# Kernel optimization log

Measured on AMD Instinct MI355X. Metric: run time of the kernel, lower is better.

The kernel has to match this reference:

```python
import jax, jax.numpy as jnp
import numpy as np

B, H, S, D = 4, 16, 2048, 64

def setup_inputs() -> dict:
    key = jax.random.key(0)
    kq, kk, kv = jax.random.split(key, 3)
    Q = jax.random.normal(kq, (B, H, S, D), dtype=jnp.float32)
    K = jax.random.normal(kk, (B, H, S, D), dtype=jnp.float32)
    V = jax.random.normal(kv, (B, H, S, D), dtype=jnp.float32)
    return {"Q": Q, "K": K, "V": V}

def reference(Q, K, V):
    # Faithful to the source: NO 1/sqrt(d) scaling.
    # scores: [B, H, S, S]
    scores = jnp.einsum("bhqd,bhkd->bhqk", Q, K)
    probs = jax.nn.softmax(scores, axis=-1)
    # output: [B, H, S, D]
    return jnp.einsum("bhqk,bhkd->bhqd", probs, V)
```

## Files before the change

kernel.cpp:

```cpp
#include <hip/hip_runtime.h>
#include <hip/hip_bf16.h>
#include <math.h>

typedef _Float16 f16x8 __attribute__((ext_vector_type(8)));
typedef _Float16 f16x4 __attribute__((ext_vector_type(4)));
typedef __fp16   hf4  __attribute__((ext_vector_type(4)));
typedef float    f32x4 __attribute__((ext_vector_type(4)));
typedef __bf16   bf16x8 __attribute__((ext_vector_type(8)));
typedef __bf16   bf16x4 __attribute__((ext_vector_type(4)));

#define MFMA32_F16(a,b,c)  __builtin_amdgcn_mfma_f32_16x16x32_f16((a),(b),(c),0,0,0)
#define MFMA_BF16(a,b,c)   __builtin_amdgcn_mfma_f32_16x16x32_bf16((a),(b),(c),0,0,0)

constexpr int S_LEN = 2048;
constexpr int DH    = 64;
constexpr int KBLK  = 64;
constexpr int NSTEP = S_LEN / KBLK;
constexpr float LOG2E = 1.44269504088896340736f;
constexpr size_t TILE_BYTES = 16384;
constexpr size_t WS_NEED = 64ull * NSTEP * TILE_BYTES;

__device__ __forceinline__ void gload16(const void* g, void* l) {
    __builtin_amdgcn_global_load_lds(
        (const __attribute__((address_space(1))) void*)g,
        (__attribute__((address_space(3))) void*)l, 16, 0, 0);
}

__device__ __forceinline__ float exp2_fast(float x) {
    float r;
    asm("v_exp_f32 %0, %1" : "=v"(r) : "v"(x));
    return r;
}

__device__ __forceinline__ float redmax_lg(float x) {
    x = fmaxf(x, __shfl_xor(x, 16));
    x = fmaxf(x, __shfl_xor(x, 32));
    return x;
}
__device__ __forceinline__ float redadd_lg(float x) {
    x += __shfl_xor(x, 16);
    x += __shfl_xor(x, 32);
    return x;
}

__device__ __forceinline__ f16x4 as_f16x4(hf4 h) {
    f16x4 f;
    __builtin_memcpy(&f, &h, 8);
    return f;
}

__global__ __launch_bounds__(256)
void prep_kernel(const float* __restrict__ Kg, const float* __restrict__ Vg,
                 unsigned char* __restrict__ ws)
{
    __shared__ _Float16 sT[64 * 70];

    const int blk = blockIdx.x;
    const int tid = threadIdx.x;
    const float* Kt = Kg + (size_t)blk * KBLK * DH;
    const float* Vt = Vg + (size_t)blk * KBLK * DH;
    char* wK = (char*)(ws + (size_t)blk * TILE_BYTES);
    char* wV = wK + 8192;

    #pragma unroll
    for (int c = 0; c < 2; ++c) {
        const int eid = tid + c * 256;
        const int row = eid >> 3;
        const int d0  = (eid & 7) * 8;
        f32x4 a = *(const f32x4*)(Kt + row * DH + d0);
        f32x4 b = *(const f32x4*)(Kt + row * DH + d0 + 4);
        f16x8 h;
        #pragma unroll
        for (int j = 0; j < 4; ++j) { h[j] = (_Float16)a[j]; h[4 + j] = (_Float16)b[j]; }
        const int koff = (row * 128 + d0 * 2) ^ ((row & 7) << 4);
        *(f16x8*)(wK + koff) = h;
        f32x4 va = *(const f32x4*)(Vt + row * DH + d0);
        f32x4 vb = *(const f32x4*)(Vt + row * DH + d0 + 4);
        #pragma unroll
        for (int j = 0; j < 4; ++j) {
            sT[row * 70 + d0 + j]     = (_Float16)va[j];
            sT[row * 70 + d0 + 4 + j] = (_Float16)vb[j];
        }
    }
    __syncthreads();
    #pragma unroll
    for (int c = 0; c < 2; ++c) {
        const int id  = tid + c * 256;
        const int p   = id >> 8;
        const int lgc = (id >> 6) & 3;
        const int d   = id & 63;
        const int kv0 = p * 32 + lgc * 4;
        f16x8 h;
        #pragma unroll
        for (int j = 0; j < 4; ++j) {
            h[j]     = sT[(kv0 + j) * 70 + d];
            h[4 + j] = sT[(kv0 + 16 + j) * 70 + d];
        }
        *(f16x8*)(wV + (p * 4 + lgc) * 1024 + d * 16) = h;
    }
}

__global__ __launch_bounds__(256, 4)
void attn_main(const float* __restrict__ Qg0, const unsigned char* __restrict__ ws,
               float* __restrict__ Og0)
{
    __shared__ __align__(16) _Float16 sK[2][KBLK * DH];
    __shared__ __align__(16) _Float16 sV[2][KBLK * DH];

    const int tid  = threadIdx.x;
    const int lane = tid & 63;
    const int w    = tid >> 6;
    const int lg   = lane >> 4;
    const int li   = lane & 15;
    const int X    = (li & 7) << 4;

    const int n   = blockIdx.x;
    const int xcd = n & 7;
    const int m_  = n >> 3;
    const int bh  = xcd * 8 + (m_ >> 4);
    const int qp  = m_ & 15;

    const float* Qg = Qg0 + (size_t)bh * S_LEN * DH;
    float*       Og = Og0 + (size_t)bh * S_LEN * DH;
    const unsigned char* wsb = ws + (size_t)bh * NSTEP * TILE_BYTES;

    f16x8 qA[2], qB[2];
    {
        const int qrowA = qp * 128 + w * 16 + li;
        const float* pa = Qg + (size_t)qrowA * DH;
        const float* pb = pa + 64 * DH;
        #pragma unroll
        for (int f = 0; f < 2; ++f) {
            f32x4 a0 = *(const f32x4*)(pa + f * 32 + lg * 8);
            f32x4 a1 = *(const f32x4*)(pa + f * 32 + lg * 8 + 4);
            f32x4 b0 = *(const f32x4*)(pb + f * 32 + lg * 8);
            f32x4 b1 = *(const f32x4*)(pb + f * 32 + lg * 8 + 4);
            #pragma unroll
            for (int j = 0; j < 4; ++j) {
                qA[f][j]     = (_Float16)(a0[j] * LOG2E);
                qA[f][4 + j] = (_Float16)(a1[j] * LOG2E);
                qB[f][j]     = (_Float16)(b0[j] * LOG2E);
                qB[f][4 + j] = (_Float16)(b1[j] * LOG2E);
            }
        }
    }

    f32x4 accoA[4], accoB[4];
    #pragma unroll
    for (int t = 0; t < 4; ++t) {
        accoA[t] = f32x4{0.f, 0.f, 0.f, 0.f};
        accoB[t] = f32x4{0.f, 0.f, 0.f, 0.f};
    }
    float mA = 0.f, lA = 0.f, mB = 0.f, lB = 0.f;

    auto stage = [&](int buf, int t) {
        const unsigned char* src = wsb + (size_t)t * TILE_BYTES;
        char* lk = (char*)&sK[buf][0] + w * 2048;
        char* lv = (char*)&sV[buf][0] + w * 2048;
        const unsigned char* gk = src + w * 2048 + lane * 16;
        const unsigned char* gv = src + 8192 + w * 2048 + lane * 16;
        gload16(gk,        lk);
        gload16(gk + 1024, lk + 1024);
        gload16(gv,        lv);
        gload16(gv + 1024, lv + 1024);
    };

    stage(0, 0);
    __syncthreads();
    int buf = 0;

    for (int t = 0; t < NSTEP; ++t) {
        if (t + 1 < NSTEP) stage(buf ^ 1, t + 1);

        const char* kb = (const char*)&sK[buf][0];
        const char* vb = (const char*)&sV[buf][0];

        f32x4 sA[4], sB[4];
        const f32x4 cA = {-mA, -mA, -mA, -mA};
        const f32x4 cB = {-mB, -mB, -mB, -mB};
        __builtin_amdgcn_s_setprio(1);
        #pragma unroll
        for (int t4 = 0; t4 < 4; ++t4) {
            const char* kr = kb + t4 * 2048 + li * 128;
            f16x8 kf0 = *(const f16x8*)(kr + ((0 * 64 + lg * 16) ^ X));
            f16x8 kf1 = *(const f16x8*)(kr + ((1 * 64 + lg * 16) ^ X));
            f32x4 a = MFMA32_F16(kf0, qA[0], cA);
            a       = MFMA32_F16(kf1, qA[1], a);
            f32x4 b = MFMA32_F16(kf0, qB[0], cB);
            b       = MFMA32_F16(kf1, qB[1], b);
            sA[t4] = a;
            sB[t4] = b;
        }
        __builtin_amdgcn_s_setprio(0);

        float mlA = fmaxf(fmaxf(fmaxf(sA[0][0], sA[0][1]), sA[0][2]),
                          fmaxf(fmaxf(sA[0][3], sA[1][0]), sA[1][1]));
        mlA = fmaxf(mlA, fmaxf(fmaxf(sA[1][2], sA[1][3]), sA[2][0]));
        mlA = fmaxf(mlA, fmaxf(fmaxf(sA[2][1], sA[2][2]), sA[2][3]));
        mlA = fmaxf(mlA, fmaxf(fmaxf(sA[3][0], sA[3][1]), fmaxf(sA[3][2], sA[3][3])));
        float mlB = fmaxf(fmaxf(fmaxf(sB[0][0], sB[0][1]), sB[0][2]),
                          fmaxf(fmaxf(sB[0][3], sB[1][0]), sB[1][1]));
        mlB = fmaxf(mlB, fmaxf(fmaxf(sB[1][2], sB[1][3]), sB[2][0]));
        mlB = fmaxf(mlB, fmaxf(fmaxf(sB[2][1], sB[2][2]), sB[2][3]));
        mlB = fmaxf(mlB, fmaxf(fmaxf(sB[3][0], sB[3][1]), fmaxf(sB[3][2], sB[3][3])));

        if (__any(mlA > 8.f)) {
            const float rowmax = redmax_lg(mlA);
            const float delta  = fmaxf(rowmax, 0.f);
            const float sc     = exp2_fast(-delta);
            mA += delta;  lA *= sc;
            #pragma unroll
            for (int t4 = 0; t4 < 4; ++t4) { accoA[t4] *= sc; sA[t4] -= delta; }
        }
        if (__any(mlB > 8.f)) {
            const float rowmax = redmax_lg(mlB);
            const float delta  = fmaxf(rowmax, 0.f);
            const float sc     = exp2_fast(-delta);
            mB += delta;  lB *= sc;
            #pragma unroll
            for (int t4 = 0; t4 < 4; ++t4) { accoB[t4] *= sc; sB[t4] -= delta; }
        }

        f16x4 pA[4], pB[4];
        float suA = 0.f, suB = 0.f;
        #pragma unroll
        for (int t4 = 0; t4 < 4; ++t4) {
            float a0 = exp2_fast(sA[t4][0]);
            float a1 = exp2_fast(sA[t4][1]);
            float a2 = exp2_fast(sA[t4][2]);
            float a3 = exp2_fast(sA[t4][3]);
            suA += (a0 + a1) + (a2 + a3);
            pA[t4] = as_f16x4(__builtin_shufflevector(
                __builtin_amdgcn_cvt_pkrtz(a0, a1),
                __builtin_amdgcn_cvt_pkrtz(a2, a3), 0, 1, 2, 3));
            float b0 = exp2_fast(sB[t4][0]);
            float b1 = exp2_fast(sB[t4][1]);
            float b2 = exp2_fast(sB[t4][2]);
            float b3 = exp2_fast(sB[t4][3]);
            suB += (b0 + b1) + (b2 + b3);
            pB[t4] = as_f16x4(__builtin_shufflevector(
                __builtin_amdgcn_cvt_pkrtz(b0, b1),
                __builtin_amdgcn_cvt_pkrtz(b2, b3), 0, 1, 2, 3));
        }
        lA += suA;
        lB += suB;

        __builtin_amdgcn_s_setprio(1);
        #pragma unroll
        for (int p = 0; p < 2; ++p) {
            f16x8 pfA = __builtin_shufflevector(pA[2 * p], pA[2 * p + 1], 0, 1, 2, 3, 4, 5, 6, 7);
            f16x8 pfB = __builtin_shufflevector(pB[2 * p], pB[2 * p + 1], 0, 1, 2, 3, 4, 5, 6, 7);
            #pragma unroll
            for (int t4v = 0; t4v < 4; ++t4v) {
                f16x8 vv = *(const f16x8*)(vb + p * 4096 + lg * 1024 + t4v * 256 + li * 16);
                accoA[t4v] = MFMA32_F16(vv, pfA, accoA[t4v]);
                accoB[t4v] = MFMA32_F16(vv, pfB, accoB[t4v]);
            }
        }
        __builtin_amdgcn_s_setprio(0);

        __syncthreads();
        buf ^= 1;
    }

    {
        const float ltotA = redadd_lg(lA);
        const float ltotB = redadd_lg(lB);
        const int qrowA = qp * 128 + w * 16 + li;
        const float ia = 1.f / ltotA;
        const float ib = 1.f / ltotB;
        float* oa = Og + (size_t)qrowA * DH;
        float* ob = oa + 64 * DH;
        #pragma unroll
        for (int t4 = 0; t4 < 4; ++t4) {
            f32x4 o1, o2;
            #pragma unroll
            for (int r = 0; r < 4; ++r) { o1[r] = accoA[t4][r] * ia; o2[r] = accoB[t4][r] * ib; }
            *(f32x4*)(oa + t4 * 16 + lg * 4) = o1;
            *(f32x4*)(ob + t4 * 16 + lg * 4) = o2;
        }
    }
}

__global__ __launch_bounds__(256)
void attn_fwd_kernel(const float* __restrict__ Qg0,
                     const float* __restrict__ Kg0,
                     const float* __restrict__ Vg0,
                     float* __restrict__ Og0)
{
    constexpr int VT_P = 72;
    constexpr int P_PB = 72;
    __shared__ __align__(16) __bf16 sKh[KBLK * DH];
    __shared__ __align__(16) __bf16 sKl[KBLK * DH];
    __shared__ __align__(16) __bf16 sVt[DH * VT_P];
    __shared__ __align__(16) __bf16 sP[4][16 * P_PB];

    const int tid  = threadIdx.x;
    const int lane = tid & 63;
    const int w    = tid >> 6;
    const int lg   = lane >> 4;
    const int li   = lane & 15;

    const int n   = blockIdx.x;
    const int xcd = n & 7;
    const int m   = n >> 3;
    const int bh  = xcd * 8 + (m >> 5);
    const int qt  = m & 31;

    const float* Qg = Qg0 + (size_t)bh * S_LEN * DH;
    const float* Kg = Kg0 + (size_t)bh * S_LEN * DH;
    const float* Vg = Vg0 + (size_t)bh * S_LEN * DH;
    float*       Og = Og0 + (size_t)bh * S_LEN * DH;

    bf16x8 qh[2], ql[2];
    {
        const int qrow = qt * 64 + w * 16 + li;
        const float* qp = Qg + (size_t)qrow * DH;
        #pragma unroll
        for (int f = 0; f < 2; ++f) {
            const int dbase = f * 32 + lg * 8;
            #pragma unroll
            for (int j = 0; j < 8; ++j) {
                float q = qp[dbase + j];
                __bf16 h = (__bf16)q;
                qh[f][j] = h;
                ql[f][j] = (__bf16)(q - (float)h);
            }
        }
    }

    f32x4 acco[4];
    #pragma unroll
    for (int t = 0; t < 4; ++t) acco[t] = f32x4{0.f, 0.f, 0.f, 0.f};
    float mval[4], lval[4];
    #pragma unroll
    for (int r = 0; r < 4; ++r) { mval[r] = -INFINITY; lval[r] = 0.f; }

    for (int step = 0; step < NSTEP; ++step) {
        __syncthreads();
        {
            const int kv0 = step * KBLK;
            #pragma unroll
            for (int i = 0; i < 4; ++i) {
                const int f4 = tid + i * 256;
                const int kv = f4 >> 4;
                const int d4 = (f4 & 15) << 2;
                f32x4 kvec = *(const f32x4*)(Kg + (size_t)(kv0 + kv) * DH + d4);
                bf16x4 h, l;
                #pragma unroll
                for (int j = 0; j < 4; ++j) {
                    __bf16 hh = (__bf16)kvec[j];
                    h[j] = hh;
                    l[j] = (__bf16)(kvec[j] - (float)hh);
                }
                const int idx = (kv * DH + d4) ^ ((kv & 7) << 3);
                *(bf16x4*)&sKh[idx] = h;
                *(bf16x4*)&sKl[idx] = l;
                f32x4 vvec = *(const f32x4*)(Vg + (size_t)(kv0 + kv) * DH + d4);
                #pragma unroll
                for (int j = 0; j < 4; ++j)
                    sVt[(d4 + j) * VT_P + kv] = (__bf16)vvec[j];
            }
        }
        __syncthreads();

        f32x4 accs[4];
        #pragma unroll
        for (int t4 = 0; t4 < 4; ++t4) {
            f32x4 acc = f32x4{0.f, 0.f, 0.f, 0.f};
            const int row = t4 * 16 + li;
            #pragma unroll
            for (int f = 0; f < 2; ++f) {
                const int idx = (row * DH + f * 32 + lg * 8) ^ ((row & 7) << 3);
                bf16x8 kh = *(const bf16x8*)&sKh[idx];
                bf16x8 kl = *(const bf16x8*)&sKl[idx];
                acc = MFMA_BF16(qh[f], kh, acc);
                acc = MFMA_BF16(qh[f], kl, acc);
                acc = MFMA_BF16(ql[f], kh, acc);
            }
            accs[t4] = acc;
        }

        #pragma unroll
        for (int r = 0; r < 4; ++r) {
            float mx = fmaxf(fmaxf(accs[0][r], accs[1][r]), fmaxf(accs[2][r], accs[3][r]));
            #pragma unroll
            for (int msk = 1; msk <= 8; msk <<= 1)
                mx = fmaxf(mx, __shfl_xor(mx, msk));
            const float newm  = fmaxf(mval[r], mx);
            const float scale = __expf(mval[r] - newm);
            mval[r] = newm;
            lval[r] *= scale;
            #pragma unroll
            for (int t4 = 0; t4 < 4; ++t4) acco[t4][r] *= scale;
            float s = 0.f;
            #pragma unroll
            for (int t4 = 0; t4 < 4; ++t4) {
                float p = __expf(accs[t4][r] - newm);
                accs[t4][r] = p;
                s += p;
            }
            #pragma unroll
            for (int msk = 1; msk <= 8; msk <<= 1)
                s += __shfl_xor(s, msk);
            lval[r] += s;
        }

        #pragma unroll
        for (int r = 0; r < 4; ++r) {
            const int rr = lg * 4 + r;
            #pragma unroll
            for (int t4 = 0; t4 < 4; ++t4)
                sP[w][rr * P_PB + t4 * 16 + li] = (__bf16)accs[t4][r];
        }

        bf16x8 pa[2];
        #pragma unroll
        for (int f = 0; f < 2; ++f)
            pa[f] = *(const bf16x8*)&sP[w][li * P_PB + f * 32 + lg * 8];
        #pragma unroll
        for (int t4 = 0; t4 < 4; ++t4) {
            #pragma unroll
            for (int f = 0; f < 2; ++f) {
                bf16x8 vb = *(const bf16x8*)&sVt[(t4 * 16 + li) * VT_P + f * 32 + lg * 8];
                acco[t4] = MFMA_BF16(pa[f], vb, acco[t4]);
            }
        }
    }

    {
        const int qrow0 = qt * 64 + w * 16;
        #pragma unroll
        for (int r = 0; r < 4; ++r) {
            const int rr = lg * 4 + r;
            const float inv = 1.f / lval[r];
            #pragma unroll
            for (int t4 = 0; t4 < 4; ++t4)
                Og[(size_t)(qrow0 + rr) * DH + t4 * 16 + li] = acco[t4][r] * inv;
        }
    }
}

extern "C" void kernel_launch(void* const* d_in, const int* in_sizes, int n_in,
                              void* d_out, int out_size, void* d_ws, size_t ws_size,
                              hipStream_t stream) {
    const float* Q = (const float*)d_in[0];
    const float* K = (const float*)d_in[1];
    const float* V = (const float*)d_in[2];
    float* O = (float*)d_out;
    if (ws_size >= WS_NEED) {
        prep_kernel<<<dim3(2048), dim3(256), 0, stream>>>(K, V, (unsigned char*)d_ws);
        attn_main<<<dim3(1024), dim3(256), 0, stream>>>(Q, (const unsigned char*)d_ws, O);
    } else {
        attn_fwd_kernel<<<dim3(2048), dim3(256), 0, stream>>>(Q, K, V, O);
    }
}
```

Before: 102.6 us.

## Software-pipeline attention loop to overlap QK^T of next tile with PV of previous

Splits the per-tile body into qkt, softmax, loadv and pv stages and reorders the loop so that each iteration computes QK^T for tile t, then PV for tile t-1, then softmax for tile t. The V fragments and packed probabilities are carried in registers across iterations, and a prologue and epilogue handle the first and last tiles. The aim is to interleave MFMA work with the exp and max softmax work so the matrix unit is less idle. In exchange it holds extra V and P registers live across iterations, which raises VGPR pressure and may reduce occupancy. The loop is also unrolled by two.

```diff
diff --git a/kernel.cpp b/kernel.cpp
--- a/kernel.cpp
+++ b/kernel.cpp
@@ -165,17 +165,10 @@
         gload16(gv + 1024, lv + 1024);
     };
 
-    stage(0, 0);
-    __syncthreads();
-    int buf = 0;
-
-    for (int t = 0; t < NSTEP; ++t) {
-        if (t + 1 < NSTEP) stage(buf ^ 1, t + 1);
-
-        const char* kb = (const char*)&sK[buf][0];
-        const char* vb = (const char*)&sV[buf][0];
-
-        f32x4 sA[4], sB[4];
+    f16x8 vprev[8];
+    f16x8 pfAprev[2], pfBprev[2];
+
+    auto qkt = [&](const char* kb, f32x4* sA, f32x4* sB) {
         const f32x4 cA = {-mA, -mA, -mA, -mA};
         const f32x4 cB = {-mB, -mB, -mB, -mB};
         __builtin_amdgcn_s_setprio(1);
@@ -192,7 +185,9 @@
             sB[t4] = b;
         }
         __builtin_amdgcn_s_setprio(0);
-
+    };
+
+    auto softmax = [&](f32x4* sA, f32x4* sB, f16x8* pfA, f16x8* pfB) {
         float mlA = fmaxf(fmaxf(fmaxf(sA[0][0], sA[0][1]), sA[0][2]),
                           fmaxf(fmaxf(sA[0][3], sA[1][0]), sA[1][1]));
         mlA = fmaxf(mlA, fmaxf(fmaxf(sA[1][2], sA[1][3]), sA[2][0]));
@@ -244,25 +239,71 @@
         }
         lA += suA;
         lB += suB;
-
+        #pragma unroll
+        for (int p = 0; p < 2; ++p) {
+            pfA[p] = __builtin_shufflevector(pA[2 * p], pA[2 * p + 1], 0, 1, 2, 3, 4, 5, 6, 7);
+            pfB[p] = __builtin_shufflevector(pB[2 * p], pB[2 * p + 1], 0, 1, 2, 3, 4, 5, 6, 7);
+        }
+    };
+
+    auto loadv = [&](const char* vb, f16x8* vv) {
+        #pragma unroll
+        for (int p = 0; p < 2; ++p)
+            #pragma unroll
+            for (int t4v = 0; t4v < 4; ++t4v)
+                vv[p * 4 + t4v] = *(const f16x8*)(vb + p * 4096 + lg * 1024 + t4v * 256 + li * 16);
+    };
+
+    auto pv = [&](const f16x8* vv, const f16x8* pfA, const f16x8* pfB) {
         __builtin_amdgcn_s_setprio(1);
         #pragma unroll
         for (int p = 0; p < 2; ++p) {
-            f16x8 pfA = __builtin_shufflevector(pA[2 * p], pA[2 * p + 1], 0, 1, 2, 3, 4, 5, 6, 7);
-            f16x8 pfB = __builtin_shufflevector(pB[2 * p], pB[2 * p + 1], 0, 1, 2, 3, 4, 5, 6, 7);
             #pragma unroll
             for (int t4v = 0; t4v < 4; ++t4v) {
-                f16x8 vv = *(const f16x8*)(vb + p * 4096 + lg * 1024 + t4v * 256 + li * 16);
-                accoA[t4v] = MFMA32_F16(vv, pfA, accoA[t4v]);
-                accoB[t4v] = MFMA32_F16(vv, pfB, accoB[t4v]);
+                accoA[t4v] = MFMA32_F16(vv[p * 4 + t4v], pfA[p], accoA[t4v]);
+                accoB[t4v] = MFMA32_F16(vv[p * 4 + t4v], pfB[p], accoB[t4v]);
             }
         }
         __builtin_amdgcn_s_setprio(0);
+    };
+
+    stage(0, 0);
+    __syncthreads();
+    int buf = 0;
+    {
+        stage(1, 1);
+        f32x4 sA[4], sB[4];
+        qkt((const char*)&sK[0][0], sA, sB);
+        loadv((const char*)&sV[0][0], vprev);
+        softmax(sA, sB, pfAprev, pfBprev);
+        __syncthreads();
+        buf = 1;
+    }
+
+    #pragma unroll 2
+    for (int t = 1; t < NSTEP; ++t) {
+        if (t + 1 < NSTEP) stage(buf ^ 1, t + 1);
+
+        f32x4 sA[4], sB[4];
+        qkt((const char*)&sK[buf][0], sA, sB);
+        pv(vprev, pfAprev, pfBprev);
+
+        f16x8 vcur[8];
+        loadv((const char*)&sV[buf][0], vcur);
+
+        f16x8 pfA[2], pfB[2];
+        softmax(sA, sB, pfA, pfB);
+
+        #pragma unroll
+        for (int i = 0; i < 8; ++i) vprev[i] = vcur[i];
+        pfAprev[0] = pfA[0]; pfAprev[1] = pfA[1];
+        pfBprev[0] = pfB[0]; pfBprev[1] = pfB[1];
 
         __syncthreads();
         buf ^= 1;
     }
 
+    pv(vprev, pfAprev, pfBprev);
     {
         const float ltotA = redadd_lg(lA);
         const float ltotB = redadd_lg(lB);
```

Result: slower. 311.3 us (+203.5%).

## Software-pipeline PV of previous tile with QK of current tile

Applied to the files above, without the earlier changes.

Restructures the attention loop so each iteration runs the P·V MFMAs for the previous key block right after the Q·K MFMAs for the current block. The softmax exponentials are then computed after both matrix phases, so the two MFMA phases can overlap with the exp/max work. V gets a third LDS buffer so the previous tile's V stays resident while the next one is being staged, and a prologue and epilogue handle the first and last tiles. This raises LDS use per block and keeps the P fragments alive across iterations, which costs registers and could lower occupancy.

```diff
diff --git a/kernel.cpp b/kernel.cpp
--- a/kernel.cpp
+++ b/kernel.cpp
@@ -105,7 +105,7 @@
                float* __restrict__ Og0)
 {
     __shared__ __align__(16) _Float16 sK[2][KBLK * DH];
-    __shared__ __align__(16) _Float16 sV[2][KBLK * DH];
+    __shared__ __align__(16) _Float16 sV[3][KBLK * DH];
 
     const int tid  = threadIdx.x;
     const int lane = tid & 63;
@@ -153,10 +153,10 @@
     }
     float mA = 0.f, lA = 0.f, mB = 0.f, lB = 0.f;
 
-    auto stage = [&](int buf, int t) {
+    auto stage = [&](char* lkb, char* lvb, int t) {
         const unsigned char* src = wsb + (size_t)t * TILE_BYTES;
-        char* lk = (char*)&sK[buf][0] + w * 2048;
-        char* lv = (char*)&sV[buf][0] + w * 2048;
+        char* lk = lkb + w * 2048;
+        char* lv = lvb + w * 2048;
         const unsigned char* gk = src + w * 2048 + lane * 16;
         const unsigned char* gv = src + 8192 + w * 2048 + lane * 16;
         gload16(gk,        lk);
@@ -165,34 +165,36 @@
         gload16(gv + 1024, lv + 1024);
     };
 
-    stage(0, 0);
+    f16x8 pfA0, pfA1, pfB0, pfB1;
+
+    char* vp = (char*)&sV[0][0];
+    char* vc = (char*)&sV[1][0];
+    char* vw = (char*)&sV[2][0];
+
+    stage((char*)&sK[0][0], vp, 0);
     __syncthreads();
-    int buf = 0;
-
-    for (int t = 0; t < NSTEP; ++t) {
-        if (t + 1 < NSTEP) stage(buf ^ 1, t + 1);
-
-        const char* kb = (const char*)&sK[buf][0];
-        const char* vb = (const char*)&sV[buf][0];
-
+    {
+        stage((char*)&sK[1][0], vc, 1);
+        const char* kb = (const char*)&sK[0][0];
         f32x4 sA[4], sB[4];
-        const f32x4 cA = {-mA, -mA, -mA, -mA};
-        const f32x4 cB = {-mB, -mB, -mB, -mB};
-        __builtin_amdgcn_s_setprio(1);
-        #pragma unroll
-        for (int t4 = 0; t4 < 4; ++t4) {
-            const char* kr = kb + t4 * 2048 + li * 128;
-            f16x8 kf0 = *(const f16x8*)(kr + ((0 * 64 + lg * 16) ^ X));
-            f16x8 kf1 = *(const f16x8*)(kr + ((1 * 64 + lg * 16) ^ X));
-            f32x4 a = MFMA32_F16(kf0, qA[0], cA);
-            a       = MFMA32_F16(kf1, qA[1], a);
-            f32x4 b = MFMA32_F16(kf0, qB[0], cB);
-            b       = MFMA32_F16(kf1, qB[1], b);
-            sA[t4] = a;
-            sB[t4] = b;
-        }
-        __builtin_amdgcn_s_setprio(0);
-
+        {
+            const f32x4 cA = {-mA, -mA, -mA, -mA};
+            const f32x4 cB = {-mB, -mB, -mB, -mB};
+            __builtin_amdgcn_s_setprio(1);
+            #pragma unroll
+            for (int t4 = 0; t4 < 4; ++t4) {
+                const char* kr = kb + t4 * 2048 + li * 128;
+                f16x8 kf0 = *(const f16x8*)(kr + ((0 * 64 + lg * 16) ^ X));
+                f16x8 kf1 = *(const f16x8*)(kr + ((1 * 64 + lg * 16) ^ X));
+                f32x4 a = MFMA32_F16(kf0, qA[0], cA);
+                a       = MFMA32_F16(kf1, qA[1], a);
+                f32x4 b = MFMA32_F16(kf0, qB[0], cB);
+                b       = MFMA32_F16(kf1, qB[1], b);
+                sA[t4] = a;
+                sB[t4] = b;
+            }
+            __builtin_amdgcn_s_setprio(0);
+        }
         float mlA = fmaxf(fmaxf(fmaxf(sA[0][0], sA[0][1]), sA[0][2]),
                           fmaxf(fmaxf(sA[0][3], sA[1][0]), sA[1][1]));
         mlA = fmaxf(mlA, fmaxf(fmaxf(sA[1][2], sA[1][3]), sA[2][0]));
@@ -244,25 +246,128 @@
         }
         lA += suA;
         lB += suB;
-
+        pfA0 = __builtin_shufflevector(pA[0], pA[1], 0, 1, 2, 3, 4, 5, 6, 7);
+        pfA1 = __builtin_shufflevector(pA[2], pA[3], 0, 1, 2, 3, 4, 5, 6, 7);
+        pfB0 = __builtin_shufflevector(pB[0], pB[1], 0, 1, 2, 3, 4, 5, 6, 7);
+        pfB1 = __builtin_shufflevector(pB[2], pB[3], 0, 1, 2, 3, 4, 5, 6, 7);
+        __syncthreads();
+    }
+
+    for (int t = 1; t < NSTEP; ++t) {
+        if (t + 1 < NSTEP) stage((char*)&sK[(t + 1) & 1][0], vw, t + 1);
+        const char* kb = (const char*)&sK[t & 1][0];
+
+        f32x4 sA[4], sB[4];
+        {
+            const f32x4 cA = {-mA, -mA, -mA, -mA};
+            const f32x4 cB = {-mB, -mB, -mB, -mB};
+            __builtin_amdgcn_s_setprio(1);
+            #pragma unroll
+            for (int t4 = 0; t4 < 4; ++t4) {
+                const char* kr = kb + t4 * 2048 + li * 128;
+                f16x8 kf0 = *(const f16x8*)(kr + ((0 * 64 + lg * 16) ^ X));
+                f16x8 kf1 = *(const f16x8*)(kr + ((1 * 64 + lg * 16) ^ X));
+                f32x4 a = MFMA32_F16(kf0, qA[0], cA);
+                a       = MFMA32_F16(kf1, qA[1], a);
+                f32x4 b = MFMA32_F16(kf0, qB[0], cB);
+                b       = MFMA32_F16(kf1, qB[1], b);
+                sA[t4] = a;
+                sB[t4] = b;
+            }
+            __builtin_amdgcn_s_setprio(0);
+        }
+
+        {
+            __builtin_amdgcn_s_setprio(1);
+            #pragma unroll
+            for (int t4v = 0; t4v < 4; ++t4v) {
+                f16x8 vv0 = *(const f16x8*)(vp + lg * 1024 + t4v * 256 + li * 16);
+                accoA[t4v] = MFMA32_F16(vv0, pfA0, accoA[t4v]);
+                accoB[t4v] = MFMA32_F16(vv0, pfB0, accoB[t4v]);
+                f16x8 vv1 = *(const f16x8*)(vp + 4096 + lg * 1024 + t4v * 256 + li * 16);
+                accoA[t4v] = MFMA32_F16(vv1, pfA1, accoA[t4v]);
+                accoB[t4v] = MFMA32_F16(vv1, pfB1, accoB[t4v]);
+            }
+            __builtin_amdgcn_s_setprio(0);
+        }
+
+        float mlA = fmaxf(fmaxf(fmaxf(sA[0][0], sA[0][1]), sA[0][2]),
+                          fmaxf(fmaxf(sA[0][3], sA[1][0]), sA[1][1]));
+        mlA = fmaxf(mlA, fmaxf(fmaxf(sA[1][2], sA[1][3]), sA[2][0]));
+        mlA = fmaxf(mlA, fmaxf(fmaxf(sA[2][1], sA[2][2]), sA[2][3]));
+        mlA = fmaxf(mlA, fmaxf(fmaxf(sA[3][0], sA[3][1]), fmaxf(sA[3][2], sA[3][3])));
+        float mlB = fmaxf(fmaxf(fmaxf(sB[0][0], sB[0][1]), sB[0][2]),
+                          fmaxf(fmaxf(sB[0][3], sB[1][0]), sB[1][1]));
+        mlB = fmaxf(mlB, fmaxf(fmaxf(sB[1][2], sB[1][3]), sB[2][0]));
+        mlB = fmaxf(mlB, fmaxf(fmaxf(sB[2][1], sB[2][2]), sB[2][3]));
+        mlB = fmaxf(mlB, fmaxf(fmaxf(sB[3][0], sB[3][1]), fmaxf(sB[3][2], sB[3][3])));
+
+        if (__any(mlA > 8.f)) {
+            const float rowmax = redmax_lg(mlA);
+            const float delta  = fmaxf(rowmax, 0.f);
+            const float sc     = exp2_fast(-delta);
+            mA += delta;  lA *= sc;
+            #pragma unroll
+            for (int t4 = 0; t4 < 4; ++t4) { accoA[t4] *= sc; sA[t4] -= delta; }
+        }
+        if (__any(mlB > 8.f)) {
+            const float rowmax = redmax_lg(mlB);
+            const float delta  = fmaxf(rowmax, 0.f);
+            const float sc     = exp2_fast(-delta);
+            mB += delta;  lB *= sc;
+            #pragma unroll
+            for (int t4 = 0; t4 < 4; ++t4) { accoB[t4] *= sc; sB[t4] -= delta; }
+        }
+
+        f16x4 pA[4], pB[4];
+        float suA = 0.f, suB = 0.f;
+        #pragma unroll
+        for (int t4 = 0; t4 < 4; ++t4) {
+            float a0 = exp2_fast(sA[t4][0]);
+            float a1 = exp2_fast(sA[t4][1]);
+            float a2 = exp2_fast(sA[t4][2]);
+            float a3 = exp2_fast(sA[t4][3]);
+            suA += (a0 + a1) + (a2 + a3);
+            pA[t4] = as_f16x4(__builtin_shufflevector(
+                __builtin_amdgcn_cvt_pkrtz(a0, a1),
+                __builtin_amdgcn_cvt_pkrtz(a2, a3), 0, 1, 2, 3));
+            float b0 = exp2_fast(sB[t4][0]);
+            float b1 = exp2_fast(sB[t4][1]);
+            float b2 = exp2_fast(sB[t4][2]);
+            float b3 = exp2_fast(sB[t4][3]);
+            suB += (b0 + b1) + (b2 + b3);
+            pB[t4] = as_f16x4(__builtin_shufflevector(
+                __builtin_amdgcn_cvt_pkrtz(b0, b1),
+                __builtin_amdgcn_cvt_pkrtz(b2, b3), 0, 1, 2, 3));
+        }
+        lA += suA;
+        lB += suB;
+        pfA0 = __builtin_shufflevector(pA[0], pA[1], 0, 1, 2, 3, 4, 5, 6, 7);
+        pfA1 = __builtin_shufflevector(pA[2], pA[3], 0, 1, 2, 3, 4, 5, 6, 7);
+        pfB0 = __builtin_shufflevector(pB[0], pB[1], 0, 1, 2, 3, 4, 5, 6, 7);
+        pfB1 = __builtin_shufflevector(pB[2], pB[3], 0, 1, 2, 3, 4, 5, 6, 7);
+
+        char* tmp = vp;
+        vp = vc;
+        vc = vw;
+        vw = tmp;
+
+        __syncthreads();
+    }
+
+    {
         __builtin_amdgcn_s_setprio(1);
         #pragma unroll
-        for (int p = 0; p < 2; ++p) {
-            f16x8 pfA = __builtin_shufflevector(pA[2 * p], pA[2 * p + 1], 0, 1, 2, 3, 4, 5, 6, 7);
-            f16x8 pfB = __builtin_shufflevector(pB[2 * p], pB[2 * p + 1], 0, 1, 2, 3, 4, 5, 6, 7);
-            #pragma unroll
-            for (int t4v = 0; t4v < 4; ++t4v) {
-                f16x8 vv = *(const f16x8*)(vb + p * 4096 + lg * 1024 + t4v * 256 + li * 16);
-                accoA[t4v] = MFMA32_F16(vv, pfA, accoA[t4v]);
-                accoB[t4v] = MFMA32_F16(vv, pfB, accoB[t4v]);
-            }
+        for (int t4v = 0; t4v < 4; ++t4v) {
+            f16x8 vv0 = *(const f16x8*)(vp + lg * 1024 + t4v * 256 + li * 16);
+            accoA[t4v] = MFMA32_F16(vv0, pfA0, accoA[t4v]);
+            accoB[t4v] = MFMA32_F16(vv0, pfB0, accoB[t4v]);
+            f16x8 vv1 = *(const f16x8*)(vp + 4096 + lg * 1024 + t4v * 256 + li * 16);
+            accoA[t4v] = MFMA32_F16(vv1, pfA1, accoA[t4v]);
+            accoB[t4v] = MFMA32_F16(vv1, pfB1, accoB[t4v]);
         }
         __builtin_amdgcn_s_setprio(0);
-
-        __syncthreads();
-        buf ^= 1;
-    }
-
+    }
     {
         const float ltotA = redadd_lg(lA);
         const float ltotB = redadd_lg(lB);
```

Result: slower. 105.2 us (+2.6%).

## Read pre-swizzled K/V fragments directly from global memory, dropping LDS staging

Applied to the files above, without the earlier changes.

The preprocessing kernel now writes K and V tiles in per-lane MFMA fragment order, so each lane's 16-byte fragment sits at chunk*1024 + lane*16. The main kernel loads these fragments straight from global/L2 memory instead of double-buffering tiles into LDS with global_load_lds and barriers. This removes LDS traffic and per-step __syncthreads, at the cost of each of the four waves and every block in the same head re-reading K/V from cache with global-load latency exposed and no explicit prefetch.

```diff
diff --git a/kernel.cpp b/kernel.cpp
--- a/kernel.cpp
+++ b/kernel.cpp
@@ -19,12 +19,6 @@
 constexpr float LOG2E = 1.44269504088896340736f;
 constexpr size_t TILE_BYTES = 16384;
 constexpr size_t WS_NEED = 64ull * NSTEP * TILE_BYTES;
-
-__device__ __forceinline__ void gload16(const void* g, void* l) {
-    __builtin_amdgcn_global_load_lds(
-        (const __attribute__((address_space(1))) void*)g,
-        (__attribute__((address_space(3))) void*)l, 16, 0, 0);
-}
 
 __device__ __forceinline__ float exp2_fast(float x) {
     float r;
@@ -72,8 +66,9 @@
         f16x8 h;
         #pragma unroll
         for (int j = 0; j < 4; ++j) { h[j] = (_Float16)a[j]; h[4 + j] = (_Float16)b[j]; }
-        const int koff = (row * 128 + d0 * 2) ^ ((row & 7) << 4);
-        *(f16x8*)(wK + koff) = h;
+        const int kchunk = (row >> 4) * 2 + (d0 >> 5);
+        const int klane  = (((d0 >> 3) & 3) << 4) | (row & 15);
+        *(f16x8*)(wK + (kchunk * 64 + klane) * 16) = h;
         f32x4 va = *(const f32x4*)(Vt + row * DH + d0);
         f32x4 vb = *(const f32x4*)(Vt + row * DH + d0 + 4);
         #pragma unroll
@@ -96,7 +91,9 @@
             h[j]     = sT[(kv0 + j) * 70 + d];
             h[4 + j] = sT[(kv0 + 16 + j) * 70 + d];
         }
-        *(f16x8*)(wV + (p * 4 + lgc) * 1024 + d * 16) = h;
+        const int vchunk = p * 4 + (d >> 4);
+        const int vlane  = (lgc << 4) | (d & 15);
+        *(f16x8*)(wV + (vchunk * 64 + vlane) * 16) = h;
     }
 }
 
@@ -104,15 +101,11 @@
 void attn_main(const float* __restrict__ Qg0, const unsigned char* __restrict__ ws,
                float* __restrict__ Og0)
 {
-    __shared__ __align__(16) _Float16 sK[2][KBLK * DH];
-    __shared__ __align__(16) _Float16 sV[2][KBLK * DH];
-
     const int tid  = threadIdx.x;
     const int lane = tid & 63;
     const int w    = tid >> 6;
     const int lg   = lane >> 4;
     const int li   = lane & 15;
-    const int X    = (li & 7) << 4;
 
     const int n   = blockIdx.x;
     const int xcd = n & 7;
@@ -153,27 +146,12 @@
     }
     float mA = 0.f, lA = 0.f, mB = 0.f, lB = 0.f;
 
-    auto stage = [&](int buf, int t) {
-        const unsigned char* src = wsb + (size_t)t * TILE_BYTES;
-        char* lk = (char*)&sK[buf][0] + w * 2048;
-        char* lv = (char*)&sV[buf][0] + w * 2048;
-        const unsigned char* gk = src + w * 2048 + lane * 16;
-        const unsigned char* gv = src + 8192 + w * 2048 + lane * 16;
-        gload16(gk,        lk);
-        gload16(gk + 1024, lk + 1024);
-        gload16(gv,        lv);
-        gload16(gv + 1024, lv + 1024);
-    };
-
-    stage(0, 0);
-    __syncthreads();
-    int buf = 0;
-
-    for (int t = 0; t < NSTEP; ++t) {
-        if (t + 1 < NSTEP) stage(buf ^ 1, t + 1);
-
-        const char* kb = (const char*)&sK[buf][0];
-        const char* vb = (const char*)&sV[buf][0];
+    const int loff = lane * 16;
+
+    const char* tp = (const char*)wsb;
+    for (int t = 0; t < NSTEP; ++t, tp += TILE_BYTES) {
+        const char* kt = tp;
+        const char* vt = tp + 8192;
 
         f32x4 sA[4], sB[4];
         const f32x4 cA = {-mA, -mA, -mA, -mA};
@@ -181,9 +159,8 @@
         __builtin_amdgcn_s_setprio(1);
         #pragma unroll
         for (int t4 = 0; t4 < 4; ++t4) {
-            const char* kr = kb + t4 * 2048 + li * 128;
-            f16x8 kf0 = *(const f16x8*)(kr + ((0 * 64 + lg * 16) ^ X));
-            f16x8 kf1 = *(const f16x8*)(kr + ((1 * 64 + lg * 16) ^ X));
+            f16x8 kf0 = *(const f16x8*)(kt + (t4 * 2 + 0) * 1024 + loff);
+            f16x8 kf1 = *(const f16x8*)(kt + (t4 * 2 + 1) * 1024 + loff);
             f32x4 a = MFMA32_F16(kf0, qA[0], cA);
             a       = MFMA32_F16(kf1, qA[1], a);
             f32x4 b = MFMA32_F16(kf0, qB[0], cB);
@@ -252,15 +229,12 @@
             f16x8 pfB = __builtin_shufflevector(pB[2 * p], pB[2 * p + 1], 0, 1, 2, 3, 4, 5, 6, 7);
             #pragma unroll
             for (int t4v = 0; t4v < 4; ++t4v) {
-                f16x8 vv = *(const f16x8*)(vb + p * 4096 + lg * 1024 + t4v * 256 + li * 16);
+                f16x8 vv = *(const f16x8*)(vt + (p * 4 + t4v) * 1024 + loff);
                 accoA[t4v] = MFMA32_F16(vv, pfA, accoA[t4v]);
                 accoB[t4v] = MFMA32_F16(vv, pfB, accoB[t4v]);
             }
         }
         __builtin_amdgcn_s_setprio(0);
-
-        __syncthreads();
-        buf ^= 1;
     }
 
     {
```

After: 130.9 us. +27.6%, slower.
